# Optimization experiments

Measured on AMD Instinct MI355X. Metric: run time of the kernel, lower is better.

The kernel has to match this reference:

```python
import jax, jax.numpy as jnp
import numpy as np

B, L, C = 32, 128, 20
TOKEN_EMBED, VOC_IV, VOC_OOEV = 300, 100000, 20000
CHAR_EMBED, CHAR_SIZE = 50, 100
NUM_FILTERS, KERNEL = 200, 3
LABELS, HID = 8, 256
NS = 6  # B,I,E,S,O,EOS states per CRF


def _lstm_dir(x, mask, w_ih, w_hh, b, reverse):
    # x: [B,L,D], mask: [B,L] -> [B,L,H]
    Bb = x.shape[0]
    Hh = w_hh.shape[1]
    xs = jnp.einsum('bld,gd->blg', x, w_ih) + b  # precompute input part [B,L,4H]
    xs_t = jnp.swapaxes(xs, 0, 1)   # [L,B,4H]
    m_t = jnp.swapaxes(mask, 0, 1)  # [L,B]
    h0 = jnp.zeros((Bb, Hh), x.dtype)

    def step(carry, inp):
        h, c = carry
        gx, m = inp
        gates = gx + h @ w_hh.T
        i, f, g, o = jnp.split(gates, 4, axis=-1)
        i = jax.nn.sigmoid(i); f = jax.nn.sigmoid(f)
        g = jnp.tanh(g); o = jax.nn.sigmoid(o)
        c_new = f * c + i * g
        h_new = o * jnp.tanh(c_new)
        mm = m[:, None]
        h = mm * h_new + (1.0 - mm) * h
        c = mm * c_new + (1.0 - mm) * c
        return (h, c), h

    _, hs = jax.lax.scan(step, (h0, h0), (xs_t, m_t), reverse=reverse)
    return jnp.swapaxes(hs, 0, 1)


def _bilstm(x, mask, layer_params):
    for (w_ih, w_hh, b) in layer_params:
        fwd = _lstm_dir(x, mask, w_ih[0], w_hh[0], b[0], False)
        bwd = _lstm_dir(x, mask, w_ih[1], w_hh[1], b[1], True)
        x = jnp.concatenate([fwd, bwd], axis=-1)
    return x


def _crf_loss(em, trans, target, mask):
    # em: [B,L,NS], trans: [NS,NS], target: [B,L] -> scalar NLL summed over batch
    em_y = jnp.take_along_axis(em, target[:, :, None], axis=2)[:, :, 0]
    tr_y = trans[target[:, :-1], target[:, 1:]]
    score = jnp.sum(em_y * mask, axis=1) + jnp.sum(tr_y * mask[:, 1:], axis=1)
    em_t = jnp.swapaxes(em, 0, 1)   # [L,B,NS]
    m_t = jnp.swapaxes(mask, 0, 1)
    alpha0 = em_t[0]

    def step(alpha, inp):
        e, m = inp
        new = jax.nn.logsumexp(alpha[:, :, None] + trans[None, :, :], axis=1) + e
        alpha = m[:, None] * new + (1.0 - m[:, None]) * alpha
        return alpha, None

    alpha, _ = jax.lax.scan(step, alpha0, (em_t[1:], m_t[1:]))
    logZ = jax.nn.logsumexp(alpha, axis=1)
    return jnp.sum(logZ - score)


def setup_inputs() -> dict:
    key = jax.random.key(0)
    ks = jax.random.split(key, 20)
    D0 = TOKEN_EMBED + NUM_FILTERS      # 500: BiLSTM layer-0 input
    D1 = 2 * HID                        # 512: BiLSTM layer-1 input
    s = 0.05
    return {
        'input_word_iv': jax.random.randint(ks[0], (B, L), 0, VOC_IV),
        'input_word_ooev': jax.random.randint(ks[1], (B, L), 0, VOC_OOEV),
        'input_char': jax.random.randint(ks[2], (B, L, C), 0, CHAR_SIZE),
        'target': jax.random.randint(ks[3], (LABELS, B, L), 0, NS),
        'mask': jnp.ones((B, L), jnp.float32),
        'embedd_word': jax.random.normal(ks[4], (VOC_IV, TOKEN_EMBED), jnp.float32) * s,
        'ooev_table': jax.random.normal(ks[5], (VOC_OOEV, TOKEN_EMBED), jnp.float32) * s,
        'char_table': jax.random.normal(ks[6], (CHAR_SIZE, CHAR_EMBED), jnp.float32) * s,
        'conv_w': jax.random.normal(ks[7], (NUM_FILTERS, CHAR_EMBED, KERNEL), jnp.float32) * s,
        'conv_b': jnp.zeros((NUM_FILTERS,), jnp.float32),
        'w_ih0': jax.random.normal(ks[8], (2, 4 * HID, D0), jnp.float32) * s,
        'w_hh0': jax.random.normal(ks[9], (2, 4 * HID, HID), jnp.float32) * s,
        'b0': jnp.zeros((2, 4 * HID), jnp.float32),
        'w_ih1': jax.random.normal(ks[10], (2, 4 * HID, D1), jnp.float32) * s,
        'w_hh1': jax.random.normal(ks[11], (2, 4 * HID, HID), jnp.float32) * s,
        'b1': jnp.zeros((2, 4 * HID), jnp.float32),
        'crf_w': jax.random.normal(ks[12], (LABELS, D1, NS), jnp.float32) * s,
        'crf_b': jnp.zeros((LABELS, NS), jnp.float32),
        'crf_trans': jax.random.normal(ks[13], (LABELS, NS, NS), jnp.float32) * s,
    }


def reference(input_word_iv, input_word_ooev, input_char, target, mask,
              embedd_word, ooev_table, char_table, conv_w, conv_b,
              w_ih0, w_hh0, b0, w_ih1, w_hh1, b1,
              crf_w, crf_b, crf_trans):
    # word embedding: frozen iv table + masked OOEV correction
    word = embedd_word[input_word_iv] \
        + (input_word_ooev != 0).astype(jnp.float32)[:, :, None] * ooev_table[input_word_ooev]
    # char CNN: masked embed -> conv1d (pad k-1 both sides) -> max-over-time -> sigmoid
    ch = (input_char != 0).astype(jnp.float32)[..., None] * char_table[input_char]  # [B,L,C,E]
    ch = ch.reshape(B * L, C, CHAR_EMBED).transpose(0, 2, 1)  # [B*L,E,C]
    conv = jax.lax.conv_general_dilated(ch, conv_w, (1,), [(KERNEL - 1, KERNEL - 1)],
                                        dimension_numbers=('NCH', 'OIH', 'NCH'))
    conv = conv + conv_b[None, :, None]
    char_feat = jax.nn.sigmoid(jnp.max(conv, axis=2)).reshape(B, L, NUM_FILTERS)
    inp = jnp.concatenate([word, char_feat], axis=2)  # [B,L,500]
    out = _bilstm(inp, mask, [(w_ih0, w_hh0, b0), (w_ih1, w_hh1, b1)])  # [B,L,512]
    # per-label CRF emissions [K,B,L,NS]
    em = jnp.einsum('bld,kdn->kbln', out, crf_w) + crf_b[:, None, None, :]
    losses = jax.vmap(_crf_loss, in_axes=(0, 0, 0, None))(em, crf_trans, target, mask)
    return jnp.sum(losses) / B
```

## Files before the change

kernel.cpp:

```cpp
#include <hip/hip_runtime.h>
#include <hip/hip_bf16.h>


typedef float floatx2 __attribute__((ext_vector_type(2)));
typedef short bf16x8 __attribute__((ext_vector_type(8)));
typedef float f32x4  __attribute__((ext_vector_type(4)));

__device__ __forceinline__ unsigned short f2bf(float x) {
    unsigned u = __float_as_uint(x);
    unsigned r = (u + 0x7fffu + ((u >> 16) & 1u)) >> 16;
    return (unsigned short)r;
}

__device__ __forceinline__ void pk_fma_bl(floatx2& acc, floatx2 w, floatx2 h) {
    asm("v_pk_fma_f32 %0, %1, %2, %0 op_sel_hi:[1,0,1]" : "+v"(acc) : "v"(w), "v"(h));
}
__device__ __forceinline__ void pk_fma_bh(floatx2& acc, floatx2 w, floatx2 h) {
    asm("v_pk_fma_f32 %0, %1, %2, %0 op_sel:[0,1,0]" : "+v"(acc) : "v"(w), "v"(h));
}

__device__ __forceinline__ float fsig(float x) {
    return __builtin_amdgcn_rcpf(1.f + __expf(-x));
}
__device__ __forceinline__ float ftanh(float x) {
    return fmaf(-2.f, __builtin_amdgcn_rcpf(1.f + __expf(2.f * x)), 1.f);
}

__device__ __forceinline__ void dot4(floatx2& aif0, floatx2& ago0,
                                     floatx2& aif1, floatx2& ago1,
                                     uint4 w, const float* hsp, int k4) {
    float4 hv = *(const float4*)(hsp + k4 * 4);
    floatx2 h01; h01.x = hv.x; h01.y = hv.y;
    floatx2 h23; h23.x = hv.z; h23.y = hv.w;
    floatx2 lo, hi;
    lo = __builtin_amdgcn_cvt_pk_f32_fp8((int)w.x, false);
    hi = __builtin_amdgcn_cvt_pk_f32_fp8((int)w.x, true);
    pk_fma_bl(aif0, lo, h01); pk_fma_bl(ago0, hi, h01);
    lo = __builtin_amdgcn_cvt_pk_f32_fp8((int)w.y, false);
    hi = __builtin_amdgcn_cvt_pk_f32_fp8((int)w.y, true);
    pk_fma_bh(aif0, lo, h01); pk_fma_bh(ago0, hi, h01);
    lo = __builtin_amdgcn_cvt_pk_f32_fp8((int)w.z, false);
    hi = __builtin_amdgcn_cvt_pk_f32_fp8((int)w.z, true);
    pk_fma_bl(aif1, lo, h23); pk_fma_bl(ago1, hi, h23);
    lo = __builtin_amdgcn_cvt_pk_f32_fp8((int)w.w, false);
    hi = __builtin_amdgcn_cvt_pk_f32_fp8((int)w.w, true);
    pk_fma_bh(aif1, lo, h23); pk_fma_bh(ago1, hi, h23);
}

__global__ void prep_misc(const float* __restrict__ wih0, const float* __restrict__ wih1,
                          const float* __restrict__ crf_w, const float* __restrict__ conv_w,
                          unsigned short* __restrict__ wbf0, unsigned short* __restrict__ wbf1,
                          float* __restrict__ crfBT, float* __restrict__ convWT,
                          float* __restrict__ outp)
{
    int idx = blockIdx.x * 256 + threadIdx.x;
    if (idx == 0) outp[0] = 0.f;
    const int NW = 2048 * 512;
    if (idx < NW) {
        int n = idx >> 9, k = idx & 511;
        wbf0[idx] = (k < 500) ? f2bf(wih0[n * 500 + k]) : (unsigned short)0;
        return;
    }
    idx -= NW;
    if (idx < NW) {
        wbf1[idx] = f2bf(wih1[idx]);
        return;
    }
    idx -= NW;
    if (idx < 48 * 512) {
        int jj = idx >> 9, d = idx & 511;
        int kL = jj / 6, n = jj % 6;
        crfBT[idx] = crf_w[(kL * 512 + d) * 6 + n];
        return;
    }
    idx -= 48 * 512;
    if (idx < 30000) {
        int f = idx % 200, ek = idx / 200;
        int e = ek / 3, kk = ek % 3;
        convWT[idx] = conv_w[(f * 50 + e) * 3 + kk];
        return;
    }
}

__global__ __launch_bounds__(256) void prep_whh(
    const float* __restrict__ wh0, const float* __restrict__ wh1,
    uint4* __restrict__ Wp0, uint4* __restrict__ Wp1)
{
    const int bid   = blockIdx.x;
    const int layer = bid >> 5;
    const int dir   = (bid >> 4) & 1;
    const int tt    = (bid >> 2) & 3;
    const int ktile = bid & 3;
    const float* w = (layer ? wh1 : wh0) + dir * 1024 * 256;
    uint4* dst = layer ? Wp1 : Wp0;
    const int t0 = tt * 64, k0 = ktile * 64;
    __shared__ float sxw[4][64][65];
    const int tid = threadIdx.x;
    #pragma unroll
    for (int g = 0; g < 4; ++g)
        #pragma unroll
        for (int q = 0; q < 4; ++q) {
            int lin = q * 256 + tid;
            int tr = lin >> 4, kc = (lin & 15) * 4;
            float4 v = *(const float4*)&w[(g * 256 + t0 + tr) * 256 + k0 + kc];
            sxw[g][tr][kc + 0] = v.x; sxw[g][tr][kc + 1] = v.y;
            sxw[g][tr][kc + 2] = v.z; sxw[g][tr][kc + 3] = v.w;
        }
    __syncthreads();
    const int t = tid & 63, k4g = tid >> 6;
    #pragma unroll
    for (int q = 0; q < 4; ++q) {
        int k4l = k4g * 4 + q;
        unsigned wrd[4];
        #pragma unroll
        for (int j = 0; j < 4; ++j) {
            int kc = k4l * 4 + j;
            float wi = sxw[0][t][kc], wf = sxw[1][t][kc];
            float wg = sxw[2][t][kc], wo = sxw[3][t][kc];
            int u = __builtin_amdgcn_cvt_pk_fp8_f32(wi, wf, 0, false);
            u     = __builtin_amdgcn_cvt_pk_fp8_f32(wg, wo, u, true);
            wrd[j] = (unsigned)u;
        }
        int k4 = (k0 >> 2) + k4l;
        dst[((size_t)dir * 64 + k4) * 256 + (t0 + t)] =
            make_uint4(wrd[0], wrd[1], wrd[2], wrd[3]);
    }
}

__global__ __launch_bounds__(256) void embed_conv(
    const int* __restrict__ iv, const int* __restrict__ ov, const int* __restrict__ ch,
    const float* __restrict__ emb, const float* __restrict__ ooev, const float* __restrict__ ctab,
    const float* __restrict__ convWT, const float* __restrict__ convB,
    unsigned short* __restrict__ inp)
{
    const int bl = blockIdx.x;
    const int tid = threadIdx.x;
    __shared__ float sx[50 * 20];
    const int ivv = iv[bl];
    const int ovv = ov[bl];
    const float mo = (ovv != 0) ? 1.f : 0.f;
    for (int e = tid; e < 300; e += 256)
        inp[bl * 512 + e] = f2bf(emb[(size_t)ivv * 300 + e] + mo * ooev[(size_t)ovv * 300 + e]);
    for (int i = tid; i < 1000; i += 256) {
        int cI = i / 50, e = i % 50;
        int id = ch[bl * 20 + cI];
        sx[e * 20 + cI] = id ? ctab[id * 50 + e] : 0.f;
    }
    if (tid >= 200 && tid < 212) inp[bl * 512 + 300 + tid] = 0;
    __syncthreads();
    if (tid < 200) {
        float acc[22];
        float bz = convB[tid];
        #pragma unroll
        for (int o = 0; o < 22; ++o) acc[o] = bz;
        for (int e = 0; e < 50; ++e) {
            float xr[20];
            #pragma unroll
            for (int q = 0; q < 5; ++q) {
                float4 v = *(const float4*)&sx[e * 20 + q * 4];
                xr[q * 4 + 0] = v.x; xr[q * 4 + 1] = v.y;
                xr[q * 4 + 2] = v.z; xr[q * 4 + 3] = v.w;
            }
            float w0 = convWT[(e * 3 + 0) * 200 + tid];
            float w1 = convWT[(e * 3 + 1) * 200 + tid];
            float w2 = convWT[(e * 3 + 2) * 200 + tid];
            #pragma unroll
            for (int o = 0; o < 22; ++o) {
                float s = acc[o];
                if (o >= 2)            s = fmaf(xr[o - 2], w0, s);
                if (o >= 1 && o <= 20) s = fmaf(xr[o - 1], w1, s);
                if (o <= 19)           s = fmaf(xr[o],     w2, s);
                acc[o] = s;
            }
        }
        float mx = acc[0];
        #pragma unroll
        for (int o = 1; o < 22; ++o) mx = fmaxf(mx, acc[o]);
        inp[bl * 512 + 300 + tid] = f2bf(1.f / (1.f + expf(-mx)));
    }
}

__global__ __launch_bounds__(256) void gemm_bf16(
    const unsigned short* __restrict__ A, const unsigned short* __restrict__ Bm,
    const float* __restrict__ bias, float* __restrict__ C, int N)
{
    __shared__ unsigned short As[4][128][8];
    __shared__ unsigned short Bs[4][128][8];
    const int tid  = threadIdx.x;
    const int wave = tid >> 6, lane = tid & 63;
    const int quad = lane >> 4, lr = lane & 15;
    const int m0 = blockIdx.y * 128, n0 = blockIdx.x * 128;

    f32x4 acc[2][8];
    #pragma unroll
    for (int mt = 0; mt < 2; ++mt)
        #pragma unroll
        for (int nt = 0; nt < 8; ++nt) acc[mt][nt] = (f32x4){0.f, 0.f, 0.f, 0.f};

    for (int kt = 0; kt < 16; ++kt) {
        #pragma unroll
        for (int p = 0; p < 2; ++p) {
            int lin = p * 256 + tid;
            int row = lin & 127, c = lin >> 7;
            *(bf16x8*)&As[c][row][0] =
                *(const bf16x8*)&A[(size_t)(m0 + row) * 512 + kt * 32 + c * 8];
            *(bf16x8*)&Bs[c][row][0] =
                *(const bf16x8*)&Bm[(size_t)(n0 + row) * 512 + kt * 32 + c * 8];
        }
        __syncthreads();
        bf16x8 bfr[8];
        #pragma unroll
        for (int nt = 0; nt < 8; ++nt)
            bfr[nt] = *(const bf16x8*)&Bs[quad][nt * 16 + lr][0];
        #pragma unroll
        for (int mt = 0; mt < 2; ++mt) {
            bf16x8 afr = *(const bf16x8*)&As[quad][wave * 32 + mt * 16 + lr][0];
            #pragma unroll
            for (int nt = 0; nt < 8; ++nt)
                acc[mt][nt] = __builtin_amdgcn_mfma_f32_16x16x32_bf16(
                    afr, bfr[nt], acc[mt][nt], 0, 0, 0);
        }
        __syncthreads();
    }
    #pragma unroll
    for (int mt = 0; mt < 2; ++mt)
        #pragma unroll
        for (int r = 0; r < 4; ++r) {
            int m = m0 + wave * 32 + mt * 16 + quad * 4 + r;
            #pragma unroll
            for (int nt = 0; nt < 8; ++nt) {
                int n = n0 + nt * 16 + lr;
                C[(size_t)m * N + n] = acc[mt][nt][r] + bias[n];
            }
        }
}

__global__ __launch_bounds__(256) void gemm_bt(
    const float* __restrict__ A, const float* __restrict__ Bm,
    const float* __restrict__ bias, float* __restrict__ C,
    int M, int N, int K)
{
    __shared__ float At[16 * 128];
    __shared__ float Bt[16 * 128];
    const int tid = threadIdx.x;
    const int tx = tid & 15, ty = tid >> 4;
    const int m0 = blockIdx.y * 128, n0 = blockIdx.x * 128;
    float acc[2][2][4][4];
    #pragma unroll
    for (int a = 0; a < 2; ++a)
        #pragma unroll
        for (int b = 0; b < 2; ++b)
            #pragma unroll
            for (int i = 0; i < 4; ++i)
                #pragma unroll
                for (int j = 0; j < 4; ++j) acc[a][b][i][j] = 0.f;

    const int lr = tid >> 2;
    const int lc = (tid & 3) << 2;
    const int ktiles = (K + 15) >> 4;
    for (int kt = 0; kt < ktiles; ++kt) {
        const int k0 = kt << 4;
        #pragma unroll
        for (int half = 0; half < 2; ++half) {
            int r = lr + half * 64;
            int gk = k0 + lc;
            {
                int gm = m0 + r;
                float4 v = make_float4(0.f, 0.f, 0.f, 0.f);
                if (gm < M) {
                    const float* p = A + (size_t)gm * K + gk;
                    if (gk + 3 < K) v = *(const float4*)p;
                    else {
                        if (gk + 0 < K) v.x = p[0];
                        if (gk + 1 < K) v.y = p[1];
                        if (gk + 2 < K) v.z = p[2];
                        if (gk + 3 < K) v.w = p[3];
                    }
                }
                At[(lc + 0) * 128 + r] = v.x; At[(lc + 1) * 128 + r] = v.y;
                At[(lc + 2) * 128 + r] = v.z; At[(lc + 3) * 128 + r] = v.w;
            }
            {
                int gn = n0 + r;
                float4 v = make_float4(0.f, 0.f, 0.f, 0.f);
                if (gn < N) {
                    const float* p = Bm + (size_t)gn * K + gk;
                    if (gk + 3 < K) v = *(const float4*)p;
                    else {
                        if (gk + 0 < K) v.x = p[0];
                        if (gk + 1 < K) v.y = p[1];
                        if (gk + 2 < K) v.z = p[2];
                        if (gk + 3 < K) v.w = p[3];
                    }
                }
                Bt[(lc + 0) * 128 + r] = v.x; Bt[(lc + 1) * 128 + r] = v.y;
                Bt[(lc + 2) * 128 + r] = v.z; Bt[(lc + 3) * 128 + r] = v.w;
            }
        }
        __syncthreads();
        #pragma unroll
        for (int k = 0; k < 16; ++k) {
            float4 a0 = *(const float4*)&At[k * 128 + (ty << 2)];
            float4 a1 = *(const float4*)&At[k * 128 + 64 + (ty << 2)];
            float4 b0 = *(const float4*)&Bt[k * 128 + (tx << 2)];
            float4 b1 = *(const float4*)&Bt[k * 128 + 64 + (tx << 2)];
            float am[2][4] = {{a0.x, a0.y, a0.z, a0.w}, {a1.x, a1.y, a1.z, a1.w}};
            float bn[2][4] = {{b0.x, b0.y, b0.z, b0.w}, {b1.x, b1.y, b1.z, b1.w}};
            #pragma unroll
            for (int qa = 0; qa < 2; ++qa)
                #pragma unroll
                for (int qb = 0; qb < 2; ++qb)
                    #pragma unroll
                    for (int i = 0; i < 4; ++i)
                        #pragma unroll
                        for (int j = 0; j < 4; ++j)
                            acc[qa][qb][i][j] = fmaf(am[qa][i], bn[qb][j], acc[qa][qb][i][j]);
        }
        __syncthreads();
    }
    #pragma unroll
    for (int qa = 0; qa < 2; ++qa)
        #pragma unroll
        for (int i = 0; i < 4; ++i) {
            int m = m0 + qa * 64 + (ty << 2) + i;
            if (m >= M) continue;
            #pragma unroll
            for (int qb = 0; qb < 2; ++qb)
                #pragma unroll
                for (int j = 0; j < 4; ++j) {
                    int n = n0 + qb * 64 + (tx << 2) + j;
                    if (n < N) C[(size_t)m * N + n] = acc[qa][qb][i][j] + bias[n];
                }
        }
}

#define L4LDS 36
__global__ __launch_bounds__(1024) void lstm_rec(
    const float* __restrict__ xs, const uint4* __restrict__ Wp,
    const float* __restrict__ mask, float* __restrict__ out,
    unsigned short* __restrict__ outb)
{
    const int tid = threadIdx.x;
    const int t   = tid & 255;
    const int kh  = tid >> 8;
    const int b   = blockIdx.x >> 1;
    const int dir = blockIdx.x & 1;
    __shared__ uint4 wlds[L4LDS * 256];
    __shared__ float4 part[3 * 256];
    __shared__ __align__(16) float hs[256];
    __shared__ float msk[128];

    const uint4* wp = Wp + (size_t)dir * 64 * 256;
    for (int j = tid; j < L4LDS * 256; j += 1024) wlds[j] = wp[j];
    if (tid < 256) hs[tid] = 0.f;
    if (tid < 128) msk[tid] = mask[b * 128 + tid];
    __syncthreads();

    const uint4* sp = wp + t;
    float h = 0.f, c = 0.f;
    for (int s = 0; s < 128; ++s) {
        const int l = dir ? (127 - s) : s;
        floatx2 aif0 = {0.f, 0.f}, ago0 = {0.f, 0.f};
        floatx2 aif1 = {0.f, 0.f}, ago1 = {0.f, 0.f};
        float gi, gf, gg2, go;
        if (kh == 0) {
            const float* gxp = xs + ((size_t)(b * 128 + l) * 2048 + dir * 1024 + t);
            gi = gxp[0]; gf = gxp[256]; gg2 = gxp[512]; go = gxp[768];
            #pragma unroll 4
            for (int k4 = 0; k4 < 13; ++k4)
                dot4(aif0, ago0, aif1, ago1, wlds[k4 * 256 + t], hs, k4);
        } else if (kh == 1) {
            uint4 a0 = sp[36 * 256], a1 = sp[37 * 256];
            uint4 a2 = sp[38 * 256], a3 = sp[39 * 256];
            #pragma unroll 4
            for (int k4 = 13; k4 < 27; ++k4)
                dot4(aif0, ago0, aif1, ago1, wlds[k4 * 256 + t], hs, k4);
            dot4(aif0, ago0, aif1, ago1, a0, hs, 36);
            dot4(aif0, ago0, aif1, ago1, a1, hs, 37);
            dot4(aif0, ago0, aif1, ago1, a2, hs, 38);
            dot4(aif0, ago0, aif1, ago1, a3, hs, 39);
        } else if (kh == 2) {
            uint4 a0 = sp[40 * 256], a1 = sp[41 * 256];
            uint4 a2 = sp[42 * 256], a3 = sp[43 * 256];
            uint4 b0 = sp[44 * 256], b1 = sp[45 * 256];
            uint4 b2 = sp[46 * 256], b3 = sp[47 * 256];
            #pragma unroll 3
            for (int k4 = 27; k4 < 36; ++k4)
                dot4(aif0, ago0, aif1, ago1, wlds[k4 * 256 + t], hs, k4);
            dot4(aif0, ago0, aif1, ago1, a0, hs, 40);
            dot4(aif0, ago0, aif1, ago1, a1, hs, 41);
            dot4(aif0, ago0, aif1, ago1, a2, hs, 42);
            dot4(aif0, ago0, aif1, ago1, a3, hs, 43);
            dot4(aif0, ago0, aif1, ago1, b0, hs, 44);
            dot4(aif0, ago0, aif1, ago1, b1, hs, 45);
            dot4(aif0, ago0, aif1, ago1, b2, hs, 46);
            dot4(aif0, ago0, aif1, ago1, b3, hs, 47);
        } else {
            uint4 a0 = sp[48 * 256], a1 = sp[49 * 256];
            uint4 a2 = sp[50 * 256], a3 = sp[51 * 256];
            uint4 b0 = sp[52 * 256], b1 = sp[53 * 256];
            uint4 b2 = sp[54 * 256], b3 = sp[55 * 256];
            dot4(aif0, ago0, aif1, ago1, a0, hs, 48);
            dot4(aif0, ago0, aif1, ago1, a1, hs, 49);
            dot4(aif0, ago0, aif1, ago1, a2, hs, 50);
            dot4(aif0, ago0, aif1, ago1, a3, hs, 51);
            a0 = sp[56 * 256]; a1 = sp[57 * 256];
            a2 = sp[58 * 256]; a3 = sp[59 * 256];
            dot4(aif0, ago0, aif1, ago1, b0, hs, 52);
            dot4(aif0, ago0, aif1, ago1, b1, hs, 53);
            dot4(aif0, ago0, aif1, ago1, b2, hs, 54);
            dot4(aif0, ago0, aif1, ago1, b3, hs, 55);
            b0 = sp[60 * 256]; b1 = sp[61 * 256];
            b2 = sp[62 * 256]; b3 = sp[63 * 256];
            dot4(aif0, ago0, aif1, ago1, a0, hs, 56);
            dot4(aif0, ago0, aif1, ago1, a1, hs, 57);
            dot4(aif0, ago0, aif1, ago1, a2, hs, 58);
            dot4(aif0, ago0, aif1, ago1, a3, hs, 59);
            dot4(aif0, ago0, aif1, ago1, b0, hs, 60);
            dot4(aif0, ago0, aif1, ago1, b1, hs, 61);
            dot4(aif0, ago0, aif1, ago1, b2, hs, 62);
            dot4(aif0, ago0, aif1, ago1, b3, hs, 63);
        }
        floatx2 aif = aif0 + aif1;
        floatx2 ago = ago0 + ago1;
        if (kh != 0)
            part[(kh - 1) * 256 + t] = make_float4(aif.x, aif.y, ago.x, ago.y);
        __syncthreads();
        if (kh == 0) {
            float4 p0 = part[t], p1 = part[256 + t], p2 = part[512 + t];
            float sai = aif.x + gi  + p0.x + p1.x + p2.x;
            float saf = aif.y + gf  + p0.y + p1.y + p2.y;
            float sag = ago.x + gg2 + p0.z + p1.z + p2.z;
            float sao = ago.y + go  + p0.w + p1.w + p2.w;
            float ig = fsig(sai);
            float fg = fsig(saf);
            float og = fsig(sao);
            float gg = ftanh(sag);
            float cn = fmaf(fg, c, ig * gg);
            float hn = og * ftanh(cn);
            float m = msk[l];
            h = m * hn + (1.f - m) * h;
            c = m * cn + (1.f - m) * c;
            hs[t] = h;
            size_t oi = (size_t)(b * 128 + l) * 512 + dir * 256 + t;
            out[oi]  = h;
            outb[oi] = f2bf(h);
        }
        __syncthreads();
    }
}
#undef L4LDS

__global__ __launch_bounds__(192) void crf_loss(
    const float* __restrict__ em, const float* __restrict__ trans,
    const int* __restrict__ target, const float* __restrict__ mask,
    float* __restrict__ outp)
{
    const int k = blockIdx.x;
    const int tid = threadIdx.x;
    const int b = tid & 31;
    const int j = tid >> 5;
    __shared__ float T[36];
    __shared__ float As[32][6];
    __shared__ float red[192];
    if (tid < 36) T[tid] = trans[k * 36 + tid];
    __syncthreads();
    const int* tg = target + (k * 32 + b) * 128;
    float sc = 0.f;
    for (int l = j; l < 128; l += 6) {
        int y = tg[l];
        float m = mask[b * 128 + l];
        sc += m * em[(b * 128 + l) * 48 + k * 6 + y];
        if (l > 0) sc += m * T[tg[l - 1] * 6 + y];
    }
    red[tid] = sc;
    float a = em[(b * 128) * 48 + k * 6 + j];
    As[b][j] = a;
    __syncthreads();
    for (int l = 1; l < 128; ++l) {
        float e = em[(b * 128 + l) * 48 + k * 6 + j];
        float v0 = As[b][0] + T[0 * 6 + j];
        float v1 = As[b][1] + T[1 * 6 + j];
        float v2 = As[b][2] + T[2 * 6 + j];
        float v3 = As[b][3] + T[3 * 6 + j];
        float v4 = As[b][4] + T[4 * 6 + j];
        float v5 = As[b][5] + T[5 * 6 + j];
        float mx = fmaxf(fmaxf(fmaxf(v0, v1), fmaxf(v2, v3)), fmaxf(v4, v5));
        float ssum = expf(v0 - mx) + expf(v1 - mx) + expf(v2 - mx)
                   + expf(v3 - mx) + expf(v4 - mx) + expf(v5 - mx);
        float na = mx + logf(ssum) + e;
        float m = mask[b * 128 + l];
        a = m * na + (1.f - m) * a;
        __syncthreads();
        As[b][j] = a;
        __syncthreads();
    }
    if (j == 0) {
        float v0 = As[b][0], v1 = As[b][1], v2 = As[b][2];
        float v3 = As[b][3], v4 = As[b][4], v5 = As[b][5];
        float mx = fmaxf(fmaxf(fmaxf(v0, v1), fmaxf(v2, v3)), fmaxf(v4, v5));
        float ssum = expf(v0 - mx) + expf(v1 - mx) + expf(v2 - mx)
                   + expf(v3 - mx) + expf(v4 - mx) + expf(v5 - mx);
        float logZ = mx + logf(ssum);
        float scb = red[b] + red[b + 32] + red[b + 64] + red[b + 96] + red[b + 128] + red[b + 160];
        red[b] = logZ - scb;
    }
    __syncthreads();
    if (tid == 0) {
        float tot = 0.f;
        for (int bb = 0; bb < 32; ++bb) tot += red[bb];
        atomicAdd(outp, tot * (1.f / 32.f));
    }
}

extern "C" void kernel_launch(void* const* d_in, const int* in_sizes, int n_in,
                              void* d_out, int out_size, void* d_ws, size_t ws_size,
                              hipStream_t stream)
{
    const int*   iv    = (const int*)d_in[0];
    const int*   ov    = (const int*)d_in[1];
    const int*   ch    = (const int*)d_in[2];
    const int*   tgt   = (const int*)d_in[3];
    const float* mask  = (const float*)d_in[4];
    const float* emb   = (const float*)d_in[5];
    const float* ooevT = (const float*)d_in[6];
    const float* ctab  = (const float*)d_in[7];
    const float* convW = (const float*)d_in[8];
    const float* convB = (const float*)d_in[9];
    const float* wih0  = (const float*)d_in[10];
    const float* whh0  = (const float*)d_in[11];
    const float* b0    = (const float*)d_in[12];
    const float* wih1  = (const float*)d_in[13];
    const float* whh1  = (const float*)d_in[14];
    const float* b1    = (const float*)d_in[15];
    const float* crfW  = (const float*)d_in[16];
    const float* crfB  = (const float*)d_in[17];
    const float* crfT  = (const float*)d_in[18];
    float* outp = (float*)d_out;

    char* ws = (char*)d_ws;
    size_t off = 0;
    auto alloc = [&](size_t bytes) {
        void* p = ws + off;
        off = (off + bytes + 255) & ~(size_t)255;
        return p;
    };
    unsigned short* inp_bf = (unsigned short*)alloc((size_t)4096 * 512 * 2);
    float* xs     = (float*)alloc((size_t)4096 * 2048 * 4);
    float* out0   = (float*)alloc((size_t)4096 * 512 * 4);
    float* out1   = (float*)alloc((size_t)4096 * 512 * 4);
    unsigned short* outb0 = (unsigned short*)alloc((size_t)4096 * 512 * 2);
    unsigned short* outb1 = (unsigned short*)alloc((size_t)4096 * 512 * 2);
    float* em     = (float*)alloc((size_t)4096 * 48 * 4);
    uint4* Wp0    = (uint4*)alloc((size_t)2 * 64 * 256 * 16);
    uint4* Wp1    = (uint4*)alloc((size_t)2 * 64 * 256 * 16);
    unsigned short* wbf0 = (unsigned short*)alloc((size_t)2048 * 512 * 2);
    unsigned short* wbf1 = (unsigned short*)alloc((size_t)2048 * 512 * 2);
    float* crfBT  = (float*)alloc((size_t)48 * 512 * 4);
    float* convWT = (float*)alloc((size_t)30000 * 4);

    const int miscN = 2 * 2048 * 512 + 48 * 512 + 30000;
    prep_misc<<<(miscN + 255) / 256, 256, 0, stream>>>(wih0, wih1, crfW, convW,
                                                       wbf0, wbf1, crfBT, convWT, outp);
    prep_whh<<<64, 256, 0, stream>>>(whh0, whh1, Wp0, Wp1);
    embed_conv<<<4096, 256, 0, stream>>>(iv, ov, ch, emb, ooevT, ctab, convWT, convB, inp_bf);
    gemm_bf16<<<dim3(16, 32), 256, 0, stream>>>(inp_bf, wbf0, b0, xs, 2048);
    lstm_rec<<<64, 1024, 0, stream>>>(xs, Wp0, mask, out0, outb0);
    gemm_bf16<<<dim3(16, 32), 256, 0, stream>>>(outb0, wbf1, b1, xs, 2048);
    lstm_rec<<<64, 1024, 0, stream>>>(xs, Wp1, mask, out1, outb1);
    gemm_bt<<<dim3(1, 32), 256, 0, stream>>>(out1, crfBT, crfB, em, 4096, 48, 512);
    crf_loss<<<8, 192, 0, stream>>>(em, crfT, tgt, mask, outp);
}
```

Before: 1.188 ms.

## Merge prep kernels, split char conv, use bf16 GEMM for CRF, repartition CRF

Merges the two weight-prep kernels into one launch, and splits the char-CNN embedding dimension across two thread halves with a shared-memory reduction. The fp32 CRF emission GEMM is replaced by the bf16 MFMA GEMM, with a padded bf16 copy of the CRF weights and a column guard on stores. The CRF loss is spread over 32 single-wave blocks, which removes the per-timestep __syncthreads. Together these aim to cut launch count and shorten serial tails, at the cost of bf16 rounding in the emissions. Inside each wave, As is written and read with no barrier, relying on lockstep wave execution.

```diff
diff --git a/kernel.cpp b/kernel.cpp
--- a/kernel.cpp
+++ b/kernel.cpp
@@ -47,13 +47,59 @@
     pk_fma_bh(aif1, lo, h23); pk_fma_bh(ago1, hi, h23);
 }
 
-__global__ void prep_misc(const float* __restrict__ wih0, const float* __restrict__ wih1,
-                          const float* __restrict__ crf_w, const float* __restrict__ conv_w,
-                          unsigned short* __restrict__ wbf0, unsigned short* __restrict__ wbf1,
-                          float* __restrict__ crfBT, float* __restrict__ convWT,
-                          float* __restrict__ outp)
-{
-    int idx = blockIdx.x * 256 + threadIdx.x;
+#define MISC_BLOCKS 8566
+__global__ __launch_bounds__(256) void prep_all(
+    const float* __restrict__ wih0, const float* __restrict__ wih1,
+    const float* __restrict__ crf_w, const float* __restrict__ conv_w,
+    const float* __restrict__ wh0, const float* __restrict__ wh1,
+    unsigned short* __restrict__ wbf0, unsigned short* __restrict__ wbf1,
+    unsigned short* __restrict__ crfbf, float* __restrict__ convWT,
+    uint4* __restrict__ Wp0, uint4* __restrict__ Wp1,
+    float* __restrict__ outp)
+{
+    __shared__ float sxw[4][64][65];
+    const int tid = threadIdx.x;
+    if (blockIdx.x >= MISC_BLOCKS) {
+        const int bid   = blockIdx.x - MISC_BLOCKS;
+        const int layer = bid >> 5;
+        const int dir   = (bid >> 4) & 1;
+        const int tt    = (bid >> 2) & 3;
+        const int ktile = bid & 3;
+        const float* w = (layer ? wh1 : wh0) + dir * 1024 * 256;
+        uint4* dst = layer ? Wp1 : Wp0;
+        const int t0 = tt * 64, k0 = ktile * 64;
+        #pragma unroll
+        for (int g = 0; g < 4; ++g)
+            #pragma unroll
+            for (int q = 0; q < 4; ++q) {
+                int lin = q * 256 + tid;
+                int tr = lin >> 4, kc = (lin & 15) * 4;
+                float4 v = *(const float4*)&w[(g * 256 + t0 + tr) * 256 + k0 + kc];
+                sxw[g][tr][kc + 0] = v.x; sxw[g][tr][kc + 1] = v.y;
+                sxw[g][tr][kc + 2] = v.z; sxw[g][tr][kc + 3] = v.w;
+            }
+        __syncthreads();
+        const int t = tid & 63, k4g = tid >> 6;
+        #pragma unroll
+        for (int q = 0; q < 4; ++q) {
+            int k4l = k4g * 4 + q;
+            unsigned wrd[4];
+            #pragma unroll
+            for (int j = 0; j < 4; ++j) {
+                int kc = k4l * 4 + j;
+                float wi = sxw[0][t][kc], wf = sxw[1][t][kc];
+                float wg = sxw[2][t][kc], wo = sxw[3][t][kc];
+                int u = __builtin_amdgcn_cvt_pk_fp8_f32(wi, wf, 0, false);
+                u     = __builtin_amdgcn_cvt_pk_fp8_f32(wg, wo, u, true);
+                wrd[j] = (unsigned)u;
+            }
+            int k4 = (k0 >> 2) + k4l;
+            dst[((size_t)dir * 64 + k4) * 256 + (t0 + t)] =
+                make_uint4(wrd[0], wrd[1], wrd[2], wrd[3]);
+        }
+        return;
+    }
+    int idx = blockIdx.x * 256 + tid;
     if (idx == 0) outp[0] = 0.f;
     const int NW = 2048 * 512;
     if (idx < NW) {
@@ -67,13 +113,17 @@
         return;
     }
     idx -= NW;
-    if (idx < 48 * 512) {
+    if (idx < 128 * 512) {
         int jj = idx >> 9, d = idx & 511;
-        int kL = jj / 6, n = jj % 6;
-        crfBT[idx] = crf_w[(kL * 512 + d) * 6 + n];
+        unsigned short v = 0;
+        if (jj < 48) {
+            int kL = jj / 6, n = jj % 6;
+            v = f2bf(crf_w[(kL * 512 + d) * 6 + n]);
+        }
+        crfbf[idx] = v;
         return;
     }
-    idx -= 48 * 512;
+    idx -= 128 * 512;
     if (idx < 30000) {
         int f = idx % 200, ek = idx / 200;
         int e = ek / 3, kk = ek % 3;
@@ -82,52 +132,7 @@
     }
 }
 
-__global__ __launch_bounds__(256) void prep_whh(
-    const float* __restrict__ wh0, const float* __restrict__ wh1,
-    uint4* __restrict__ Wp0, uint4* __restrict__ Wp1)
-{
-    const int bid   = blockIdx.x;
-    const int layer = bid >> 5;
-    const int dir   = (bid >> 4) & 1;
-    const int tt    = (bid >> 2) & 3;
-    const int ktile = bid & 3;
-    const float* w = (layer ? wh1 : wh0) + dir * 1024 * 256;
-    uint4* dst = layer ? Wp1 : Wp0;
-    const int t0 = tt * 64, k0 = ktile * 64;
-    __shared__ float sxw[4][64][65];
-    const int tid = threadIdx.x;
-    #pragma unroll
-    for (int g = 0; g < 4; ++g)
-        #pragma unroll
-        for (int q = 0; q < 4; ++q) {
-            int lin = q * 256 + tid;
-            int tr = lin >> 4, kc = (lin & 15) * 4;
-            float4 v = *(const float4*)&w[(g * 256 + t0 + tr) * 256 + k0 + kc];
-            sxw[g][tr][kc + 0] = v.x; sxw[g][tr][kc + 1] = v.y;
-            sxw[g][tr][kc + 2] = v.z; sxw[g][tr][kc + 3] = v.w;
-        }
-    __syncthreads();
-    const int t = tid & 63, k4g = tid >> 6;
-    #pragma unroll
-    for (int q = 0; q < 4; ++q) {
-        int k4l = k4g * 4 + q;
-        unsigned wrd[4];
-        #pragma unroll
-        for (int j = 0; j < 4; ++j) {
-            int kc = k4l * 4 + j;
-            float wi = sxw[0][t][kc], wf = sxw[1][t][kc];
-            float wg = sxw[2][t][kc], wo = sxw[3][t][kc];
-            int u = __builtin_amdgcn_cvt_pk_fp8_f32(wi, wf, 0, false);
-            u     = __builtin_amdgcn_cvt_pk_fp8_f32(wg, wo, u, true);
-            wrd[j] = (unsigned)u;
-        }
-        int k4 = (k0 >> 2) + k4l;
-        dst[((size_t)dir * 64 + k4) * 256 + (t0 + t)] =
-            make_uint4(wrd[0], wrd[1], wrd[2], wrd[3]);
-    }
-}
-
-__global__ __launch_bounds__(256) void embed_conv(
+__global__ __launch_bounds__(512) void embed_conv(
     const int* __restrict__ iv, const int* __restrict__ ov, const int* __restrict__ ch,
     const float* __restrict__ emb, const float* __restrict__ ooev, const float* __restrict__ ctab,
     const float* __restrict__ convWT, const float* __restrict__ convB,
@@ -136,24 +141,27 @@
     const int bl = blockIdx.x;
     const int tid = threadIdx.x;
     __shared__ float sx[50 * 20];
+    __shared__ float pc[200][22];
     const int ivv = iv[bl];
     const int ovv = ov[bl];
     const float mo = (ovv != 0) ? 1.f : 0.f;
-    for (int e = tid; e < 300; e += 256)
-        inp[bl * 512 + e] = f2bf(emb[(size_t)ivv * 300 + e] + mo * ooev[(size_t)ovv * 300 + e]);
-    for (int i = tid; i < 1000; i += 256) {
+    if (tid < 300)
+        inp[bl * 512 + tid] = f2bf(emb[(size_t)ivv * 300 + tid] + mo * ooev[(size_t)ovv * 300 + tid]);
+    if (tid >= 500) inp[bl * 512 + tid] = 0;
+    for (int i = tid; i < 1000; i += 512) {
         int cI = i / 50, e = i % 50;
         int id = ch[bl * 20 + cI];
         sx[e * 20 + cI] = id ? ctab[id * 50 + e] : 0.f;
     }
-    if (tid >= 200 && tid < 212) inp[bl * 512 + 300 + tid] = 0;
     __syncthreads();
-    if (tid < 200) {
-        float acc[22];
-        float bz = convB[tid];
-        #pragma unroll
-        for (int o = 0; o < 22; ++o) acc[o] = bz;
-        for (int e = 0; e < 50; ++e) {
+    const int f = tid & 255, eh = tid >> 8;
+    float acc[22];
+    if (f < 200) {
+        float init = eh ? 0.f : convB[f];
+        #pragma unroll
+        for (int o = 0; o < 22; ++o) acc[o] = init;
+        const int e0 = eh * 25;
+        for (int e = e0; e < e0 + 25; ++e) {
             float xr[20];
             #pragma unroll
             for (int q = 0; q < 5; ++q) {
@@ -161,9 +169,9 @@
                 xr[q * 4 + 0] = v.x; xr[q * 4 + 1] = v.y;
                 xr[q * 4 + 2] = v.z; xr[q * 4 + 3] = v.w;
             }
-            float w0 = convWT[(e * 3 + 0) * 200 + tid];
-            float w1 = convWT[(e * 3 + 1) * 200 + tid];
-            float w2 = convWT[(e * 3 + 2) * 200 + tid];
+            float w0 = convWT[(e * 3 + 0) * 200 + f];
+            float w1 = convWT[(e * 3 + 1) * 200 + f];
+            float w2 = convWT[(e * 3 + 2) * 200 + f];
             #pragma unroll
             for (int o = 0; o < 22; ++o) {
                 float s = acc[o];
@@ -173,16 +181,23 @@
                 acc[o] = s;
             }
         }
-        float mx = acc[0];
-        #pragma unroll
-        for (int o = 1; o < 22; ++o) mx = fmaxf(mx, acc[o]);
-        inp[bl * 512 + 300 + tid] = f2bf(1.f / (1.f + expf(-mx)));
+        if (eh) {
+            #pragma unroll
+            for (int o = 0; o < 22; ++o) pc[f][o] = acc[o];
+        }
+    }
+    __syncthreads();
+    if (f < 200 && eh == 0) {
+        float mx = acc[0] + pc[f][0];
+        #pragma unroll
+        for (int o = 1; o < 22; ++o) mx = fmaxf(mx, acc[o] + pc[f][o]);
+        inp[bl * 512 + 300 + f] = f2bf(1.f / (1.f + expf(-mx)));
     }
 }
 
 __global__ __launch_bounds__(256) void gemm_bf16(
     const unsigned short* __restrict__ A, const unsigned short* __restrict__ Bm,
-    const float* __restrict__ bias, float* __restrict__ C, int N)
+    const float* __restrict__ bias, float* __restrict__ C, int ldC, int Nguard)
 {
     __shared__ unsigned short As[4][128][8];
     __shared__ unsigned short Bs[4][128][8];
@@ -230,107 +245,8 @@
             #pragma unroll
             for (int nt = 0; nt < 8; ++nt) {
                 int n = n0 + nt * 16 + lr;
-                C[(size_t)m * N + n] = acc[mt][nt][r] + bias[n];
+                if (n < Nguard) C[(size_t)m * ldC + n] = acc[mt][nt][r] + bias[n];
             }
-        }
-}
-
-__global__ __launch_bounds__(256) void gemm_bt(
-    const float* __restrict__ A, const float* __restrict__ Bm,
-    const float* __restrict__ bias, float* __restrict__ C,
-    int M, int N, int K)
-{
-    __shared__ float At[16 * 128];
-    __shared__ float Bt[16 * 128];
-    const int tid = threadIdx.x;
-    const int tx = tid & 15, ty = tid >> 4;
-    const int m0 = blockIdx.y * 128, n0 = blockIdx.x * 128;
-    float acc[2][2][4][4];
-    #pragma unroll
-    for (int a = 0; a < 2; ++a)
-        #pragma unroll
-        for (int b = 0; b < 2; ++b)
-            #pragma unroll
-            for (int i = 0; i < 4; ++i)
-                #pragma unroll
-                for (int j = 0; j < 4; ++j) acc[a][b][i][j] = 0.f;
-
-    const int lr = tid >> 2;
-    const int lc = (tid & 3) << 2;
-    const int ktiles = (K + 15) >> 4;
-    for (int kt = 0; kt < ktiles; ++kt) {
-        const int k0 = kt << 4;
-        #pragma unroll
-        for (int half = 0; half < 2; ++half) {
-            int r = lr + half * 64;
-            int gk = k0 + lc;
-            {
-                int gm = m0 + r;
-                float4 v = make_float4(0.f, 0.f, 0.f, 0.f);
-                if (gm < M) {
-                    const float* p = A + (size_t)gm * K + gk;
-                    if (gk + 3 < K) v = *(const float4*)p;
-                    else {
-                        if (gk + 0 < K) v.x = p[0];
-                        if (gk + 1 < K) v.y = p[1];
-                        if (gk + 2 < K) v.z = p[2];
-                        if (gk + 3 < K) v.w = p[3];
-                    }
-                }
-                At[(lc + 0) * 128 + r] = v.x; At[(lc + 1) * 128 + r] = v.y;
-                At[(lc + 2) * 128 + r] = v.z; At[(lc + 3) * 128 + r] = v.w;
-            }
-            {
-                int gn = n0 + r;
-                float4 v = make_float4(0.f, 0.f, 0.f, 0.f);
-                if (gn < N) {
-                    const float* p = Bm + (size_t)gn * K + gk;
-                    if (gk + 3 < K) v = *(const float4*)p;
-                    else {
-                        if (gk + 0 < K) v.x = p[0];
-                        if (gk + 1 < K) v.y = p[1];
-                        if (gk + 2 < K) v.z = p[2];
-                        if (gk + 3 < K) v.w = p[3];
-                    }
-                }
-                Bt[(lc + 0) * 128 + r] = v.x; Bt[(lc + 1) * 128 + r] = v.y;
-                Bt[(lc + 2) * 128 + r] = v.z; Bt[(lc + 3) * 128 + r] = v.w;
-            }
-        }
-        __syncthreads();
-        #pragma unroll
-        for (int k = 0; k < 16; ++k) {
-            float4 a0 = *(const float4*)&At[k * 128 + (ty << 2)];
-            float4 a1 = *(const float4*)&At[k * 128 + 64 + (ty << 2)];
-            float4 b0 = *(const float4*)&Bt[k * 128 + (tx << 2)];
-            float4 b1 = *(const float4*)&Bt[k * 128 + 64 + (tx << 2)];
-            float am[2][4] = {{a0.x, a0.y, a0.z, a0.w}, {a1.x, a1.y, a1.z, a1.w}};
-            float bn[2][4] = {{b0.x, b0.y, b0.z, b0.w}, {b1.x, b1.y, b1.z, b1.w}};
-            #pragma unroll
-            for (int qa = 0; qa < 2; ++qa)
-                #pragma unroll
-                for (int qb = 0; qb < 2; ++qb)
-                    #pragma unroll
-                    for (int i = 0; i < 4; ++i)
-                        #pragma unroll
-                        for (int j = 0; j < 4; ++j)
-                            acc[qa][qb][i][j] = fmaf(am[qa][i], bn[qb][j], acc[qa][qb][i][j]);
-        }
-        __syncthreads();
-    }
-    #pragma unroll
-    for (int qa = 0; qa < 2; ++qa)
-        #pragma unroll
-        for (int i = 0; i < 4; ++i) {
-            int m = m0 + qa * 64 + (ty << 2) + i;
-            if (m >= M) continue;
-            #pragma unroll
-            for (int qb = 0; qb < 2; ++qb)
-                #pragma unroll
-                for (int j = 0; j < 4; ++j) {
-                    int n = n0 + qb * 64 + (tx << 2) + j;
-                    if (n < N) C[(size_t)m * N + n] = acc[qa][qb][i][j] + bias[n];
-                }
         }
 }
 
@@ -451,65 +367,66 @@
 }
 #undef L4LDS
 
-__global__ __launch_bounds__(192) void crf_loss(
+__global__ __launch_bounds__(64) void crf_loss(
     const float* __restrict__ em, const float* __restrict__ trans,
     const int* __restrict__ target, const float* __restrict__ mask,
     float* __restrict__ outp)
 {
-    const int k = blockIdx.x;
+    const int k  = blockIdx.x >> 2;
+    const int bq = blockIdx.x & 3;
     const int tid = threadIdx.x;
-    const int b = tid & 31;
-    const int j = tid >> 5;
     __shared__ float T[36];
-    __shared__ float As[32][6];
-    __shared__ float red[192];
+    __shared__ float As[8][6];
+    __shared__ float red[48];
+    __shared__ float res[8];
     if (tid < 36) T[tid] = trans[k * 36 + tid];
-    __syncthreads();
-    const int* tg = target + (k * 32 + b) * 128;
-    float sc = 0.f;
-    for (int l = j; l < 128; l += 6) {
-        int y = tg[l];
-        float m = mask[b * 128 + l];
-        sc += m * em[(b * 128 + l) * 48 + k * 6 + y];
-        if (l > 0) sc += m * T[tg[l - 1] * 6 + y];
-    }
-    red[tid] = sc;
-    float a = em[(b * 128) * 48 + k * 6 + j];
-    As[b][j] = a;
-    __syncthreads();
-    for (int l = 1; l < 128; ++l) {
-        float e = em[(b * 128 + l) * 48 + k * 6 + j];
-        float v0 = As[b][0] + T[0 * 6 + j];
-        float v1 = As[b][1] + T[1 * 6 + j];
-        float v2 = As[b][2] + T[2 * 6 + j];
-        float v3 = As[b][3] + T[3 * 6 + j];
-        float v4 = As[b][4] + T[4 * 6 + j];
-        float v5 = As[b][5] + T[5 * 6 + j];
-        float mx = fmaxf(fmaxf(fmaxf(v0, v1), fmaxf(v2, v3)), fmaxf(v4, v5));
-        float ssum = expf(v0 - mx) + expf(v1 - mx) + expf(v2 - mx)
-                   + expf(v3 - mx) + expf(v4 - mx) + expf(v5 - mx);
-        float na = mx + logf(ssum) + e;
-        float m = mask[b * 128 + l];
-        a = m * na + (1.f - m) * a;
-        __syncthreads();
-        As[b][j] = a;
-        __syncthreads();
-    }
-    if (j == 0) {
-        float v0 = As[b][0], v1 = As[b][1], v2 = As[b][2];
-        float v3 = As[b][3], v4 = As[b][4], v5 = As[b][5];
-        float mx = fmaxf(fmaxf(fmaxf(v0, v1), fmaxf(v2, v3)), fmaxf(v4, v5));
-        float ssum = expf(v0 - mx) + expf(v1 - mx) + expf(v2 - mx)
-                   + expf(v3 - mx) + expf(v4 - mx) + expf(v5 - mx);
-        float logZ = mx + logf(ssum);
-        float scb = red[b] + red[b + 32] + red[b + 64] + red[b + 96] + red[b + 128] + red[b + 160];
-        red[b] = logZ - scb;
-    }
-    __syncthreads();
-    if (tid == 0) {
-        float tot = 0.f;
-        for (int bb = 0; bb < 32; ++bb) tot += red[bb];
-        atomicAdd(outp, tot * (1.f / 32.f));
+    if (tid < 48) {
+        const int bloc = tid / 6;
+        const int j    = tid - bloc * 6;
+        const int b    = bq * 8 + bloc;
+        const int* tg = target + (k * 32 + b) * 128;
+        float sc = 0.f;
+        for (int l = j; l < 128; l += 6) {
+            int y = tg[l];
+            float m = mask[b * 128 + l];
+            sc += m * em[(b * 128 + l) * 48 + k * 6 + y];
+            if (l > 0) sc += m * T[tg[l - 1] * 6 + y];
+        }
+        red[tid] = sc;
+        float a = em[(b * 128) * 48 + k * 6 + j];
+        As[bloc][j] = a;
+        for (int l = 1; l < 128; ++l) {
+            float e = em[(b * 128 + l) * 48 + k * 6 + j];
+            float v0 = As[bloc][0] + T[0 * 6 + j];
+            float v1 = As[bloc][1] + T[1 * 6 + j];
+            float v2 = As[bloc][2] + T[2 * 6 + j];
+            float v3 = As[bloc][3] + T[3 * 6 + j];
+            float v4 = As[bloc][4] + T[4 * 6 + j];
+            float v5 = As[bloc][5] + T[5 * 6 + j];
+            float mx = fmaxf(fmaxf(fmaxf(v0, v1), fmaxf(v2, v3)), fmaxf(v4, v5));
+            float ssum = expf(v0 - mx) + expf(v1 - mx) + expf(v2 - mx)
+                       + expf(v3 - mx) + expf(v4 - mx) + expf(v5 - mx);
+            float na = mx + logf(ssum) + e;
+            float m = mask[b * 128 + l];
+            a = m * na + (1.f - m) * a;
+            As[bloc][j] = a;
+        }
+        if (j == 0) {
+            float v0 = As[bloc][0], v1 = As[bloc][1], v2 = As[bloc][2];
+            float v3 = As[bloc][3], v4 = As[bloc][4], v5 = As[bloc][5];
+            float mx = fmaxf(fmaxf(fmaxf(v0, v1), fmaxf(v2, v3)), fmaxf(v4, v5));
+            float ssum = expf(v0 - mx) + expf(v1 - mx) + expf(v2 - mx)
+                       + expf(v3 - mx) + expf(v4 - mx) + expf(v5 - mx);
+            float logZ = mx + logf(ssum);
+            float scb = red[bloc * 6 + 0] + red[bloc * 6 + 1] + red[bloc * 6 + 2]
+                      + red[bloc * 6 + 3] + red[bloc * 6 + 4] + red[bloc * 6 + 5];
+            res[bloc] = logZ - scb;
+        }
+        if (tid == 0) {
+            float tot = res[0] + res[1] + res[2] + res[3]
+                      + res[4] + res[5] + res[6] + res[7];
+            atomicAdd(outp, tot * (1.f / 32.f));
+        }
     }
 }
 
@@ -556,18 +473,17 @@
     uint4* Wp1    = (uint4*)alloc((size_t)2 * 64 * 256 * 16);
     unsigned short* wbf0 = (unsigned short*)alloc((size_t)2048 * 512 * 2);
     unsigned short* wbf1 = (unsigned short*)alloc((size_t)2048 * 512 * 2);
-    float* crfBT  = (float*)alloc((size_t)48 * 512 * 4);
+    unsigned short* crfbf = (unsigned short*)alloc((size_t)128 * 512 * 2);
     float* convWT = (float*)alloc((size_t)30000 * 4);
 
-    const int miscN = 2 * 2048 * 512 + 48 * 512 + 30000;
-    prep_misc<<<(miscN + 255) / 256, 256, 0, stream>>>(wih0, wih1, crfW, convW,
-                                                       wbf0, wbf1, crfBT, convWT, outp);
-    prep_whh<<<64, 256, 0, stream>>>(whh0, whh1, Wp0, Wp1);
-    embed_conv<<<4096, 256, 0, stream>>>(iv, ov, ch, emb, ooevT, ctab, convWT, convB, inp_bf);
-    gemm_bf16<<<dim3(16, 32), 256, 0, stream>>>(inp_bf, wbf0, b0, xs, 2048);
+    prep_all<<<MISC_BLOCKS + 64, 256, 0, stream>>>(
+        wih0, wih1, crfW, convW, whh0, whh1,
+        wbf0, wbf1, crfbf, convWT, Wp0, Wp1, outp);
+    embed_conv<<<4096, 512, 0, stream>>>(iv, ov, ch, emb, ooevT, ctab, convWT, convB, inp_bf);
+    gemm_bf16<<<dim3(16, 32), 256, 0, stream>>>(inp_bf, wbf0, b0, xs, 2048, 2048);
     lstm_rec<<<64, 1024, 0, stream>>>(xs, Wp0, mask, out0, outb0);
-    gemm_bf16<<<dim3(16, 32), 256, 0, stream>>>(outb0, wbf1, b1, xs, 2048);
+    gemm_bf16<<<dim3(16, 32), 256, 0, stream>>>(outb0, wbf1, b1, xs, 2048, 2048);
     lstm_rec<<<64, 1024, 0, stream>>>(xs, Wp1, mask, out1, outb1);
-    gemm_bt<<<dim3(1, 32), 256, 0, stream>>>(out1, crfBT, crfB, em, 4096, 48, 512);
-    crf_loss<<<8, 192, 0, stream>>>(em, crfT, tgt, mask, outp);
-}
+    gemm_bf16<<<dim3(1, 32), 256, 0, stream>>>(outb1, crfbf, crfB, em, 48, 48);
+    crf_loss<<<32, 64, 0, stream>>>(em, crfT, tgt, mask, outp);
+}
```

Measured after the change: 1.195 ms. About the same (+0.5%).
